# Optimization experiments

Hardware: AMD Instinct MI355X
Metric: run time of the kernel (lower is better)

## Reference

```python
import jax, jax.numpy as jnp
import numpy as np
from jax import lax

N, C_IN, H, W = 32, 128, 64, 64
C_OUT, KH, KW = 256, 3, 3
C_DIM = 64


def setup_inputs() -> dict:
    key = jax.random.key(0)
    k1, k2, k3, k4, k5 = jax.random.split(key, 5)
    return {
        "x": jax.random.normal(k1, (N, C_IN, H, W), dtype=jnp.float32),
        "c": jax.random.normal(k2, (N, C_DIM), dtype=jnp.float32),
        "weight": jax.random.normal(k3, (C_OUT, C_IN, KH, KW), dtype=jnp.float32),
        "c_weight": jax.random.normal(k4, (C_OUT, C_DIM), dtype=jnp.float32),
        "bias": jax.random.normal(k5, (C_OUT,), dtype=jnp.float32),
    }


def reference(x, c, weight, c_weight, bias):
    # Equivalent to the module's unfold + matmul path (groups=1, dilation=1,
    # zero padding=1, stride=1): a direct conv fused with the spatially
    # invariant context bias c @ c_weight^T and the channel bias.
    out = lax.conv_general_dilated(
        x, weight,
        window_strides=(1, 1),
        padding=((1, 1), (1, 1)),
        dimension_numbers=("NCHW", "OIHW", "NCHW"),
    )  # (N, C_out, H, W)
    ctx = jnp.einsum("nd,od->no", c, c_weight)  # (N, C_out), same at every spatial loc
    return out + ctx[:, :, None, None] + bias[None, :, None, None]
```

## Files before the change

### kernel.cpp

```cpp
#include <hip/hip_runtime.h>
#include <hip/hip_bf16.h>


#define NN   32
#define CIN  128
#define HH   64
#define WW   64
#define COUT 256
#define CDIM 64
#define HP   66
#define WP   66

#define XP_BYTES  ((size_t)NN*HP*WP*CIN*2)
#define WT_BYTES  ((size_t)9*COUT*CIN*2)
#define CTX_BYTES ((size_t)NN*COUT*4)
#define WS_NEEDED (XP_BYTES + WT_BYTES + CTX_BYTES)

typedef __attribute__((ext_vector_type(8))) short short8;
typedef __attribute__((ext_vector_type(4))) float float4v;

__device__ __forceinline__ void async16(const void* g, void* l) {
    __builtin_amdgcn_global_load_lds(
        (const __attribute__((address_space(1))) unsigned int*)g,
        (__attribute__((address_space(3))) unsigned int*)l, 16, 0, 0);
}

#define BAR()      __builtin_amdgcn_s_barrier()
#define SETPRIO(x) __builtin_amdgcn_s_setprio(x)

__global__ __launch_bounds__(256) void prep_all(
    const float* __restrict__ x, const float* __restrict__ c,
    const float* __restrict__ wgt, const float* __restrict__ cw,
    const float* __restrict__ bias,
    __hip_bfloat16* __restrict__ xP, __hip_bfloat16* __restrict__ wT,
    float* __restrict__ ctx)
{
    __shared__ float tile[CIN][65];
    int bid = blockIdx.x;
    int t   = threadIdx.x;

    if (bid < 2048) {
        int n = bid >> 6;
        int h = bid & 63;
        const float* xb = x + (size_t)n * CIN * HH * WW + (size_t)h * WW;

        int lane16 = t & 15, rgrp = t >> 4;
        #pragma unroll
        for (int i = 0; i < 8; ++i) {
            int ci = rgrp + i * 16;
            float4v v = *(const float4v*)(xb + (size_t)ci * (HH * WW) + lane16 * 4);
            int w0 = lane16 * 4;
            tile[ci][w0]     = v.x;
            tile[ci][w0 + 1] = v.y;
            tile[ci][w0 + 2] = v.z;
            tile[ci][w0 + 3] = v.w;
        }
        __syncthreads();

        int oct = t & 3, w = t >> 2;
        __hip_bfloat16* db = xP + (((size_t)n * HP + (h + 1)) * WP + (w + 1)) * CIN;
        #pragma unroll
        for (int p = 0; p < 4; ++p) {
            int ci0 = p * 32 + oct * 8;
            union { short8 v; __hip_bfloat16 b[8]; } u;
            #pragma unroll
            for (int j = 0; j < 8; ++j)
                u.b[j] = __float2bfloat16(tile[ci0 + j][w]);
            *(short8*)(db + ci0) = u.v;
        }
    } else if (bid < 2568) {
        int g = (bid - 2048) * 256 + t;
        int n   = g / 4160;
        int rem = g - n * 4160;
        int pi  = rem >> 4;
        int oct = rem & 15;
        int hh, ww;
        if (pi < 132) { hh = (pi >= 66) ? 65 : 0; ww = pi % 66; }
        else { int p2 = pi - 132; ww = (p2 >= 64) ? 65 : 0; hh = 1 + (p2 & 63); }
        short8 z = {};
        *(short8*)(xP + (((size_t)n * HP + hh) * WP + ww) * CIN + oct * 8) = z;
    } else {
        int b2 = bid - 2568;
        if (b2 < 1152) {
            int idx = b2 * 256 + t;
            int ci  = idx & 127;
            int co  = (idx >> 7) & 255;
            int tap = idx >> 15;
            wT[idx] = __float2bfloat16(wgt[((size_t)co * CIN + ci) * 9 + tap]);
        } else {
            int idx = (b2 - 1152) * 256 + t;
            int co = idx & 255, n = idx >> 8;
            float a = bias[co];
            #pragma unroll 8
            for (int d = 0; d < CDIM; ++d) a += c[n * CDIM + d] * cw[co * CDIM + d];
            ctx[idx] = a;
        }
    }
}

__global__ __launch_bounds__(512) void conv_mfma(
    const __hip_bfloat16* __restrict__ xP,
    const __hip_bfloat16* __restrict__ wT,
    const float* __restrict__ ctx,
    float* __restrict__ out)
{
    __shared__ __align__(16) short A_s[50688];
    __shared__ __align__(16) short B_s[3][8192];

    int bid = blockIdx.x;
    int mt  = (bid & 7) * 64 + (bid >> 3);
    int n   = mt >> 4;
    int h0  = (mt & 15) << 2;

    int tid  = threadIdx.x;
    int lane = tid & 63, wv = tid >> 6;
    int wm = (wv & 1) * 128;
    int wn = (wv >> 1) * 64;
    int l15 = lane & 15, lu = lane >> 4;

    const __hip_bfloat16* xPn = xP + (size_t)(n * HP + h0) * WP * CIN;
    #pragma unroll
    for (int rnd = 0; rnd < 13; ++rnd) {
        int g = rnd * 512 + tid;
        if (g < 6336) {
            int r  = g >> 4, cc = g & 15;
            int hh = r / 66;
            int ww = r - hh * 66;
            int so = ((cc & 7) ^ (r & 7)) | (cc & 8);
            async16(xPn + ((size_t)hh * WP + ww) * CIN + so * 8, &A_s[g * 8]);
        }
    }

    int coS = tid >> 2, clS = tid & 3;
    int soS = clS ^ ((coS >> 1) & 3);
    const __hip_bfloat16* bsrc0 = wT + (size_t)coS * CIN + soS * 8;

    #pragma unroll
    for (int b = 0; b < 2; ++b) {
        const __hip_bfloat16* bs = bsrc0 + b * 32;
        async16(bs,             &B_s[b][tid * 8]);
        async16(bs + 128 * CIN, &B_s[b][(512 + tid) * 8]);
    }
    asm volatile("s_waitcnt vmcnt(2)" ::: "memory");

    int ohc = wm >> 6;
    int pbB = lu ^ ((l15 >> 1) & 3);

    float4v acc[8][4] = {};

    #pragma unroll 3
    for (int kt = 0; kt < 36; ++kt) {
        BAR();

        if (kt < 34) {
            int t2 = kt + 2, tap2 = t2 >> 2, kb2 = t2 & 3;
            const __hip_bfloat16* bs = bsrc0 + (size_t)tap2 * (COUT * CIN) + kb2 * 32;
            short* Bd = &B_s[(kt + 2) % 3][0];
            async16(bs,             Bd + tid * 8);
            async16(bs + 128 * CIN, Bd + (512 + tid) * 8);
        }

        int tap = kt >> 2, kb = kt & 3;
        int kh  = (tap * 11) >> 5, kw = tap - kh * 3;
        int rb0 = (ohc + kh) * 66 + l15 + kw;
        int cL  = kb * 4 + lu;
        int c7  = cL & 7, cg = cL & 8;
        const short* Bb = &B_s[kt % 3][0];

        short8 aF[8], bF[4];
        #pragma unroll
        for (int mi = 0; mi < 8; ++mi) {
            int r    = rb0 + (mi >> 2) * 66 + (mi & 3) * 16;
            int phys = (c7 ^ (r & 7)) | cg;
            aF[mi] = *(const short8*)&A_s[r * 128 + phys * 8];
        }
        #pragma unroll
        for (int ni = 0; ni < 4; ++ni) {
            int co = wn + ni * 16 + l15;
            bF[ni] = *(const short8*)&Bb[co * 32 + pbB * 8];
        }

        SETPRIO(1);
        #pragma unroll
        for (int mi = 0; mi < 8; ++mi)
            #pragma unroll
            for (int ni = 0; ni < 4; ++ni)
                acc[mi][ni] = __builtin_amdgcn_mfma_f32_16x16x32_bf16(
                    aF[mi], bF[ni], acc[mi][ni], 0, 0, 0);
        SETPRIO(0);

        if (kt < 34) asm volatile("s_waitcnt vmcnt(2)" ::: "memory");
        else         asm volatile("s_waitcnt vmcnt(0)" ::: "memory");
    }

    #pragma unroll
    for (int ni = 0; ni < 4; ++ni) {
        int co = wn + ni * 16 + l15;
        float cv = ctx[n * COUT + co];
        float* ob = out + ((size_t)n * COUT + co) * (HH * WW);
        #pragma unroll
        for (int mi = 0; mi < 8; ++mi) {
            int rp = wm + mi * 16 + (lu << 2);
            int hh = h0 + (rp >> 6);
            int ww = rp & 63;
            float4v v = acc[mi][ni] + cv;
            *(float4v*)&ob[hh * WW + ww] = v;
        }
    }
}

__global__ __launch_bounds__(256) void contextual_conv_f32(
    const float* __restrict__ x, const float* __restrict__ c,
    const float* __restrict__ wgt, const float* __restrict__ cw,
    const float* __restrict__ bias, float* __restrict__ out)
{
    int idx = blockIdx.x * 256 + threadIdx.x;
    int w = idx & 63, h = (idx >> 6) & 63, cb = (idx >> 12) & 63, n = idx >> 18;
    float acc[4];
    #pragma unroll
    for (int j = 0; j < 4; ++j) acc[j] = bias[cb + j * 64];
    const float* cp = c + n * CDIM;
    for (int d = 0; d < CDIM; ++d) {
        float cv = cp[d];
        #pragma unroll
        for (int j = 0; j < 4; ++j) acc[j] += cv * cw[(cb + j * 64) * CDIM + d];
    }
    const float* xn = x + (size_t)n * (CIN * HH * WW);
    for (int ci = 0; ci < CIN; ++ci) {
        const float* xc = xn + ci * (HH * WW);
        float wv[4][9];
        #pragma unroll
        for (int j = 0; j < 4; ++j) {
            const float* wp = wgt + ((cb + j * 64) * CIN + ci) * 9;
            #pragma unroll
            for (int k = 0; k < 9; ++k) wv[j][k] = wp[k];
        }
        #pragma unroll
        for (int kh = 0; kh < 3; ++kh) {
            int hh = h + kh - 1;
            if (hh < 0 || hh >= HH) continue;
            const float* xr = xc + hh * WW;
            #pragma unroll
            for (int kw = 0; kw < 3; ++kw) {
                int ww = w + kw - 1;
                if (ww < 0 || ww >= WW) continue;
                float xv = xr[ww];
                #pragma unroll
                for (int j = 0; j < 4; ++j) acc[j] += xv * wv[j][kh * 3 + kw];
            }
        }
    }
    size_t obase = (size_t)n * (COUT * HH * WW) + (size_t)h * WW + w;
    #pragma unroll
    for (int j = 0; j < 4; ++j)
        out[obase + (size_t)(cb + j * 64) * (HH * WW)] = acc[j];
}

extern "C" void kernel_launch(void* const* d_in, const int* in_sizes, int n_in,
                              void* d_out, int out_size, void* d_ws, size_t ws_size,
                              hipStream_t stream) {
    const float* x    = (const float*)d_in[0];
    const float* c    = (const float*)d_in[1];
    const float* wgt  = (const float*)d_in[2];
    const float* cw   = (const float*)d_in[3];
    const float* bias = (const float*)d_in[4];
    float* out = (float*)d_out;

    if (ws_size < WS_NEEDED) {
        const int total_threads = NN * 64 * HH * WW;
        contextual_conv_f32<<<total_threads / 256, 256, 0, stream>>>(x, c, wgt, cw, bias, out);
        return;
    }

    char* ws = (char*)d_ws;
    __hip_bfloat16* xP = (__hip_bfloat16*)ws;
    __hip_bfloat16* wT = (__hip_bfloat16*)(ws + XP_BYTES);
    float*          cx = (float*)(ws + XP_BYTES + WT_BYTES);

    prep_all <<<3752, 256, 0, stream>>>(x, c, wgt, cw, bias, xP, wT, cx);
    conv_mfma<<<512, 512, 0, stream>>>(xP, wT, cx, out);
}
```

Baseline: 270.3 us.

## Load conv weights directly from global into registers, drop LDS B staging

Removes the triple-buffered LDS staging of weight tiles and the per-k-step barrier. Each wave now loads its B fragments straight from global memory (cached in L2) into registers, prefetching the next step while the current MFMAs run. With the B buffers gone, shared memory per block shrinks, and launch bounds request 2 blocks per SM. The cost is redundant global loads of weights across waves and possible register pressure from double-buffered fragments under the tighter occupancy bound.

```diff
diff --git a/kernel.cpp b/kernel.cpp
--- a/kernel.cpp
+++ b/kernel.cpp
@@ -25,7 +25,6 @@
         (__attribute__((address_space(3))) unsigned int*)l, 16, 0, 0);
 }
 
-#define BAR()      __builtin_amdgcn_s_barrier()
 #define SETPRIO(x) __builtin_amdgcn_s_setprio(x)
 
 __global__ __launch_bounds__(256) void prep_all(
@@ -98,14 +97,13 @@
     }
 }
 
-__global__ __launch_bounds__(512) void conv_mfma(
+__global__ __launch_bounds__(512, 2) void conv_mfma(
     const __hip_bfloat16* __restrict__ xP,
     const __hip_bfloat16* __restrict__ wT,
     const float* __restrict__ ctx,
     float* __restrict__ out)
 {
     __shared__ __align__(16) short A_s[50688];
-    __shared__ __align__(16) short B_s[3][8192];
 
     int bid = blockIdx.x;
     int mt  = (bid & 7) * 64 + (bid >> 3);
@@ -131,66 +129,54 @@
         }
     }
 
-    int coS = tid >> 2, clS = tid & 3;
-    int soS = clS ^ ((coS >> 1) & 3);
-    const __hip_bfloat16* bsrc0 = wT + (size_t)coS * CIN + soS * 8;
-
-    #pragma unroll
-    for (int b = 0; b < 2; ++b) {
-        const __hip_bfloat16* bs = bsrc0 + b * 32;
-        async16(bs,             &B_s[b][tid * 8]);
-        async16(bs + 128 * CIN, &B_s[b][(512 + tid) * 8]);
-    }
-    asm volatile("s_waitcnt vmcnt(2)" ::: "memory");
+    const __hip_bfloat16* wB = wT + ((size_t)(wn + l15) * CIN) + lu * 8;
+
+    short8 bCur[4], bNxt[4];
+    #pragma unroll
+    for (int ni = 0; ni < 4; ++ni)
+        bCur[ni] = *(const short8*)(wB + (size_t)ni * (16 * CIN));
+
+    __syncthreads();
 
     int ohc = wm >> 6;
-    int pbB = lu ^ ((l15 >> 1) & 3);
-
     float4v acc[8][4] = {};
 
-    #pragma unroll 3
-    for (int kt = 0; kt < 36; ++kt) {
-        BAR();
-
-        if (kt < 34) {
-            int t2 = kt + 2, tap2 = t2 >> 2, kb2 = t2 & 3;
-            const __hip_bfloat16* bs = bsrc0 + (size_t)tap2 * (COUT * CIN) + kb2 * 32;
-            short* Bd = &B_s[(kt + 2) % 3][0];
-            async16(bs,             Bd + tid * 8);
-            async16(bs + 128 * CIN, Bd + (512 + tid) * 8);
-        }
-
-        int tap = kt >> 2, kb = kt & 3;
+    for (int tap = 0; tap < 9; ++tap) {
         int kh  = (tap * 11) >> 5, kw = tap - kh * 3;
         int rb0 = (ohc + kh) * 66 + l15 + kw;
-        int cL  = kb * 4 + lu;
-        int c7  = cL & 7, cg = cL & 8;
-        const short* Bb = &B_s[kt % 3][0];
-
-        short8 aF[8], bF[4];
-        #pragma unroll
-        for (int mi = 0; mi < 8; ++mi) {
-            int r    = rb0 + (mi >> 2) * 66 + (mi & 3) * 16;
-            int phys = (c7 ^ (r & 7)) | cg;
-            aF[mi] = *(const short8*)&A_s[r * 128 + phys * 8];
-        }
-        #pragma unroll
-        for (int ni = 0; ni < 4; ++ni) {
-            int co = wn + ni * 16 + l15;
-            bF[ni] = *(const short8*)&Bb[co * 32 + pbB * 8];
-        }
-
-        SETPRIO(1);
-        #pragma unroll
-        for (int mi = 0; mi < 8; ++mi)
+        #pragma unroll
+        for (int kb = 0; kb < 4; ++kb) {
+            int s1 = tap * 4 + kb + 1;
+            if (s1 > 35) s1 = 0;
+            int tap1 = s1 >> 2, kb1 = s1 & 3;
+            const __hip_bfloat16* wNx = wB + (size_t)tap1 * (COUT * CIN) + kb1 * 32;
             #pragma unroll
             for (int ni = 0; ni < 4; ++ni)
-                acc[mi][ni] = __builtin_amdgcn_mfma_f32_16x16x32_bf16(
-                    aF[mi], bF[ni], acc[mi][ni], 0, 0, 0);
-        SETPRIO(0);
-
-        if (kt < 34) asm volatile("s_waitcnt vmcnt(2)" ::: "memory");
-        else         asm volatile("s_waitcnt vmcnt(0)" ::: "memory");
+                bNxt[ni] = *(const short8*)(wNx + (size_t)ni * (16 * CIN));
+
+            int cL = kb * 4 + lu;
+            int c7 = cL & 7;
+            int cg = (cL & 8) << 3;
+            short8 aF[8];
+            #pragma unroll
+            for (int mi = 0; mi < 8; ++mi) {
+                int r    = rb0 + (mi >> 2) * 66 + (mi & 3) * 16;
+                int phys = c7 ^ (r & 7);
+                aF[mi] = *(const short8*)&A_s[r * 128 + cg + phys * 8];
+            }
+
+            SETPRIO(1);
+            #pragma unroll
+            for (int mi = 0; mi < 8; ++mi)
+                #pragma unroll
+                for (int ni = 0; ni < 4; ++ni)
+                    acc[mi][ni] = __builtin_amdgcn_mfma_f32_16x16x32_bf16(
+                        aF[mi], bCur[ni], acc[mi][ni], 0, 0, 0);
+            SETPRIO(0);
+
+            #pragma unroll
+            for (int ni = 0; ni < 4; ++ni) bCur[ni] = bNxt[ni];
+        }
     }
 
     #pragma unroll
```

Result: no change. 270.6 us (+0.1%).
